# Kernel optimization log

Measured on AMD Instinct MI355X. Metric: run time of the kernel, lower is better.

The kernel has to match this reference:

```python
import jax, jax.numpy as jnp
import numpy as np

EPS = 1e-5
N, K, C = 200000, 9, 64  # active sites, 3x3 kernel offsets, channels


def setup_inputs() -> dict:
    key = jax.random.key(0)
    ks = jax.random.split(key, 4)
    x = jax.random.normal(ks[0], (N, C), dtype=jnp.float32)
    # rulebook: neighbor index per active site per kernel offset (submanifold conv)
    nbr = jax.random.randint(ks[1], (N, K), 0, N, dtype=jnp.int32)
    W1 = jax.random.normal(ks[2], (K, C, C), dtype=jnp.float32) * 0.05
    W2 = jax.random.normal(ks[3], (K, C, C), dtype=jnp.float32) * 0.05
    ones = jnp.ones((C,), dtype=jnp.float32)
    zeros = jnp.zeros((C,), dtype=jnp.float32)
    return {
        'x': x, 'nbr': nbr,
        'W1': W1, 'g1': ones, 'b1': zeros, 'rm1': zeros, 'rv1': ones,
        'W2': W2, 'g2': ones, 'b2': zeros, 'rm2': zeros, 'rv2': ones,
    }


def _subm_conv(f, nbr, W):
    # gather neighbor features [N, K, C] then contract with [K, C, C]
    return jnp.einsum('nkc,kcd->nd', f[nbr], W)


def _bn(a, g, b, rm, rv):
    inv = g * jax.lax.rsqrt(rv + EPS)
    return a * inv + (b - rm * inv)


def reference(x, nbr, W1, g1, b1, rm1, rv1, W2, g2, b2, rm2, rv2):
    a = _subm_conv(x, nbr, W1)
    a = jax.nn.relu(_bn(a, g1, b1, rm1, rv1))
    a = _subm_conv(a, nbr, W2)
    a = _bn(a, g2, b2, rm2, rv2)
    return jax.nn.relu(a + x)
```

## Files before the change

### kernel.cpp

```cpp
#include <hip/hip_runtime.h>

#define EPS 1e-5f

typedef unsigned short ushort;
typedef unsigned int uint;
typedef __attribute__((ext_vector_type(8)))  short  short8;
typedef __attribute__((ext_vector_type(8)))  ushort ushort8;
typedef __attribute__((ext_vector_type(16))) float  f32x16;

__device__ __forceinline__ ushort f2bf(float v) {
    uint b = __float_as_uint(v);
    return (ushort)((b + 0x7fffu + ((b >> 16) & 1u)) >> 16);
}
__device__ __forceinline__ float bf2f(ushort u) {
    return __uint_as_float(((uint)u) << 16);
}

__global__ void prep_w(const float* __restrict__ W,
                       ushort* __restrict__ hi, ushort* __restrict__ lo) {
    int e = blockIdx.x * 256 + threadIdx.x;
    int c = e & 63, d = (e >> 6) & 63, k = e >> 12;
    float v = W[(k << 12) + (c << 6) + d];
    ushort h = f2bf(v);
    hi[e] = h;
    lo[e] = f2bf(v - bf2f(h));
}

template<bool SECOND>
__global__ __launch_bounds__(256, 4) void subm_conv_mfma(
    const float*  __restrict__ f,
    const int*    __restrict__ nbr,
    const ushort* __restrict__ Wth,
    const ushort* __restrict__ Wtl,
    const float*  __restrict__ gamma,
    const float*  __restrict__ beta,
    const float*  __restrict__ rmean,
    const float*  __restrict__ rvar,
    const float*  __restrict__ resid,
    float* __restrict__ out)
{
    __shared__ __align__(16) ushort Ah[64][72];
    __shared__ __align__(16) ushort Al[64][72];
    __shared__ __align__(16) ushort Bh[64][72];
    __shared__ __align__(16) ushort Bl[64][72];

    const int t    = threadIdx.x;
    const int lane = t & 63;
    const int w    = t >> 6;
    const int wr   = (w >> 1) << 5;
    const int wc   = (w & 1) << 5;
    const int row0 = blockIdx.x << 6;

    const int sr = t >> 2;
    const int sc = (t & 3) << 4;

    f32x16 acc = 0.f;

    const int rA   = wr + (lane & 31);
    const int rB   = wc + (lane & 31);
    const int koff = (lane >> 5) << 3;

    for (int k = 0; k < 9; ++k) {
        const int m = nbr[(row0 + sr) * 9 + k];
        const float4* ap = (const float4*)(f + (size_t)m * 64 + sc);
        float4 v0 = ap[0], v1 = ap[1], v2 = ap[2], v3 = ap[3];

        const int woff = (k << 12) + (sr << 6) + sc;
        const uint4* whp = (const uint4*)(Wth + woff);
        const uint4* wlp = (const uint4*)(Wtl + woff);
        uint4 wh0 = whp[0], wh1 = whp[1];
        uint4 wl0 = wlp[0], wl1 = wlp[1];

        float a0[8] = {v0.x,v0.y,v0.z,v0.w, v1.x,v1.y,v1.z,v1.w};
        float a1[8] = {v2.x,v2.y,v2.z,v2.w, v3.x,v3.y,v3.z,v3.w};
        ushort8 h0, l0, h1, l1;
        #pragma unroll
        for (int j = 0; j < 8; ++j) {
            ushort h = f2bf(a0[j]);
            h0[j] = h; l0[j] = f2bf(a0[j] - bf2f(h));
            ushort g = f2bf(a1[j]);
            h1[j] = g; l1[j] = f2bf(a1[j] - bf2f(g));
        }

        __syncthreads();

        *(ushort8*)&Ah[sr][sc]     = h0;
        *(ushort8*)&Al[sr][sc]     = l0;
        *(ushort8*)&Ah[sr][sc + 8] = h1;
        *(ushort8*)&Al[sr][sc + 8] = l1;
        *(uint4*)&Bh[sr][sc]       = wh0;
        *(uint4*)&Bh[sr][sc + 8]   = wh1;
        *(uint4*)&Bl[sr][sc]       = wl0;
        *(uint4*)&Bl[sr][sc + 8]   = wl1;

        __syncthreads();

        #pragma unroll
        for (int h = 0; h < 4; ++h) {
            const int co = (h << 4) + koff;
            short8 fah = *(const short8*)&Ah[rA][co];
            short8 fal = *(const short8*)&Al[rA][co];
            short8 fbh = *(const short8*)&Bh[rB][co];
            short8 fbl = *(const short8*)&Bl[rB][co];
            acc = __builtin_amdgcn_mfma_f32_32x32x16_bf16(fah, fbh, acc, 0, 0, 0);
            acc = __builtin_amdgcn_mfma_f32_32x32x16_bf16(fah, fbl, acc, 0, 0, 0);
            acc = __builtin_amdgcn_mfma_f32_32x32x16_bf16(fal, fbh, acc, 0, 0, 0);
        }
    }

    const int d   = wc + (lane & 31);
    const float iv  = gamma[d] * rsqrtf(rvar[d] + EPS);
    const float add = beta[d] - rmean[d] * iv;
    const int rb  = row0 + wr + ((lane >> 5) << 2);
    #pragma unroll
    for (int i = 0; i < 16; ++i) {
        const int n = rb + (i & 3) + ((i >> 2) << 3);
        float val = fmaf(acc[i], iv, add);
        if (SECOND) val += resid[(size_t)n * 64 + d];
        out[(size_t)n * 64 + d] = fmaxf(val, 0.f);
    }
}

extern "C" void kernel_launch(void* const* d_in, const int* in_sizes, int n_in,
                              void* d_out, int out_size, void* d_ws, size_t ws_size,
                              hipStream_t stream) {
    const float* x   = (const float*)d_in[0];
    const int*   nbr = (const int*)  d_in[1];
    const float* W1  = (const float*)d_in[2];
    const float* g1  = (const float*)d_in[3];
    const float* b1  = (const float*)d_in[4];
    const float* rm1 = (const float*)d_in[5];
    const float* rv1 = (const float*)d_in[6];
    const float* W2  = (const float*)d_in[7];
    const float* g2  = (const float*)d_in[8];
    const float* b2  = (const float*)d_in[9];
    const float* rm2 = (const float*)d_in[10];
    const float* rv2 = (const float*)d_in[11];

    const int N    = in_sizes[0] / 64;
    const int grid = N / 64;

    char* ws = (char*)d_ws;
    float*  mid  = (float*)ws;                         ws += (size_t)N * 64 * 4;
    ushort* W1h  = (ushort*)ws;                        ws += 9 * 64 * 64 * 2;
    ushort* W1l  = (ushort*)ws;                        ws += 9 * 64 * 64 * 2;
    ushort* W2h  = (ushort*)ws;                        ws += 9 * 64 * 64 * 2;
    ushort* W2l  = (ushort*)ws;

    prep_w<<<144, 256, 0, stream>>>(W1, W1h, W1l);
    prep_w<<<144, 256, 0, stream>>>(W2, W2h, W2l);

    subm_conv_mfma<false><<<grid, 256, 0, stream>>>(
        x,   nbr, W1h, W1l, g1, b1, rm1, rv1, nullptr, mid);
    subm_conv_mfma<true ><<<grid, 256, 0, stream>>>(
        mid, nbr, W2h, W2l, g2, b2, rm2, rv2, x, (float*)d_out);
}
```

Baseline: 273.1 us.

## Pre-swizzle weights into MFMA fragment order and load B directly from global

The weight prep kernel now writes the bf16 hi/lo weights in the exact per-lane MFMA B-fragment order, and both weight tensors are prepared in one launch. The conv kernel drops the B tiles from shared memory and reads its B fragments straight from global/L2 with 16-byte loads, which halves LDS usage and removes the weight staging stores. Launch bounds rise from 4 to 8 blocks per CU to use the freed LDS for occupancy. In exchange the MFMA loop now waits on global loads of weights, which should stay cache-resident, and register pressure under the tighter bound may force spills.

```diff
diff --git a/kernel.cpp b/kernel.cpp
--- a/kernel.cpp
+++ b/kernel.cpp
@@ -16,22 +16,28 @@
     return __uint_as_float(((uint)u) << 16);
 }
 
-__global__ void prep_w(const float* __restrict__ W,
-                       ushort* __restrict__ hi, ushort* __restrict__ lo) {
+__global__ void prep_w2(const float* __restrict__ W1, const float* __restrict__ W2,
+                        ushort* __restrict__ h1, ushort* __restrict__ l1,
+                        ushort* __restrict__ h2, ushort* __restrict__ l2) {
     int e = blockIdx.x * 256 + threadIdx.x;
-    int c = e & 63, d = (e >> 6) & 63, k = e >> 12;
-    float v = W[(k << 12) + (c << 6) + d];
-    ushort h = f2bf(v);
-    hi[e] = h;
-    lo[e] = f2bf(v - bf2f(h));
+    const float* W = W1; ushort* ho = h1; ushort* lo = l1;
+    if (e >= 36864) { e -= 36864; W = W2; ho = h2; lo = l2; }
+    const int j = e & 7, l = (e >> 3) & 63, h = (e >> 9) & 3,
+              wc2 = (e >> 11) & 1, k = e >> 12;
+    const int d = wc2 * 32 + (l & 31);
+    const int c = h * 16 + ((l >> 5) << 3) + j;
+    const float v = W[(k << 12) + (c << 6) + d];
+    const ushort hh = f2bf(v);
+    ho[e] = hh;
+    lo[e] = f2bf(v - bf2f(hh));
 }
 
 template<bool SECOND>
-__global__ __launch_bounds__(256, 4) void subm_conv_mfma(
+__global__ __launch_bounds__(256, 8) void subm_conv_mfma(
     const float*  __restrict__ f,
     const int*    __restrict__ nbr,
-    const ushort* __restrict__ Wth,
-    const ushort* __restrict__ Wtl,
+    const ushort* __restrict__ Wfh,
+    const ushort* __restrict__ Wfl,
     const float*  __restrict__ gamma,
     const float*  __restrict__ beta,
     const float*  __restrict__ rmean,
@@ -41,14 +47,12 @@
 {
     __shared__ __align__(16) ushort Ah[64][72];
     __shared__ __align__(16) ushort Al[64][72];
-    __shared__ __align__(16) ushort Bh[64][72];
-    __shared__ __align__(16) ushort Bl[64][72];
 
     const int t    = threadIdx.x;
     const int lane = t & 63;
     const int w    = t >> 6;
     const int wr   = (w >> 1) << 5;
-    const int wc   = (w & 1) << 5;
+    const int wc2  = w & 1;
     const int row0 = blockIdx.x << 6;
 
     const int sr = t >> 2;
@@ -57,19 +61,12 @@
     f32x16 acc = 0.f;
 
     const int rA   = wr + (lane & 31);
-    const int rB   = wc + (lane & 31);
     const int koff = (lane >> 5) << 3;
 
     for (int k = 0; k < 9; ++k) {
         const int m = nbr[(row0 + sr) * 9 + k];
         const float4* ap = (const float4*)(f + (size_t)m * 64 + sc);
         float4 v0 = ap[0], v1 = ap[1], v2 = ap[2], v3 = ap[3];
-
-        const int woff = (k << 12) + (sr << 6) + sc;
-        const uint4* whp = (const uint4*)(Wth + woff);
-        const uint4* wlp = (const uint4*)(Wtl + woff);
-        uint4 wh0 = whp[0], wh1 = whp[1];
-        uint4 wl0 = wlp[0], wl1 = wlp[1];
 
         float a0[8] = {v0.x,v0.y,v0.z,v0.w, v1.x,v1.y,v1.z,v1.w};
         float a1[8] = {v2.x,v2.y,v2.z,v2.w, v3.x,v3.y,v3.z,v3.w};
@@ -88,30 +85,28 @@
         *(ushort8*)&Al[sr][sc]     = l0;
         *(ushort8*)&Ah[sr][sc + 8] = h1;
         *(ushort8*)&Al[sr][sc + 8] = l1;
-        *(uint4*)&Bh[sr][sc]       = wh0;
-        *(uint4*)&Bh[sr][sc + 8]   = wh1;
-        *(uint4*)&Bl[sr][sc]       = wl0;
-        *(uint4*)&Bl[sr][sc + 8]   = wl1;
 
         __syncthreads();
 
+        const ushort* bh = Wfh + (((k * 2 + wc2) * 4) * 64 + lane) * 8;
+        const ushort* bl = Wfl + (((k * 2 + wc2) * 4) * 64 + lane) * 8;
         #pragma unroll
         for (int h = 0; h < 4; ++h) {
             const int co = (h << 4) + koff;
             short8 fah = *(const short8*)&Ah[rA][co];
             short8 fal = *(const short8*)&Al[rA][co];
-            short8 fbh = *(const short8*)&Bh[rB][co];
-            short8 fbl = *(const short8*)&Bl[rB][co];
+            short8 fbh = *(const short8*)(bh + (h << 9));
+            short8 fbl = *(const short8*)(bl + (h << 9));
             acc = __builtin_amdgcn_mfma_f32_32x32x16_bf16(fah, fbh, acc, 0, 0, 0);
             acc = __builtin_amdgcn_mfma_f32_32x32x16_bf16(fah, fbl, acc, 0, 0, 0);
             acc = __builtin_amdgcn_mfma_f32_32x32x16_bf16(fal, fbh, acc, 0, 0, 0);
         }
     }
 
-    const int d   = wc + (lane & 31);
+    const int d     = (wc2 << 5) + (lane & 31);
     const float iv  = gamma[d] * rsqrtf(rvar[d] + EPS);
     const float add = beta[d] - rmean[d] * iv;
-    const int rb  = row0 + wr + ((lane >> 5) << 2);
+    const int rb    = row0 + wr + ((lane >> 5) << 2);
     #pragma unroll
     for (int i = 0; i < 16; ++i) {
         const int n = rb + (i & 3) + ((i >> 2) << 3);
@@ -141,14 +136,13 @@
     const int grid = N / 64;
 
     char* ws = (char*)d_ws;
-    float*  mid  = (float*)ws;                         ws += (size_t)N * 64 * 4;
-    ushort* W1h  = (ushort*)ws;                        ws += 9 * 64 * 64 * 2;
-    ushort* W1l  = (ushort*)ws;                        ws += 9 * 64 * 64 * 2;
-    ushort* W2h  = (ushort*)ws;                        ws += 9 * 64 * 64 * 2;
-    ushort* W2l  = (ushort*)ws;
+    float*  mid = (float*)ws;            ws += (size_t)N * 64 * 4;
+    ushort* W1h = (ushort*)ws;           ws += 36864 * 2;
+    ushort* W1l = (ushort*)ws;           ws += 36864 * 2;
+    ushort* W2h = (ushort*)ws;           ws += 36864 * 2;
+    ushort* W2l = (ushort*)ws;
 
-    prep_w<<<144, 256, 0, stream>>>(W1, W1h, W1l);
-    prep_w<<<144, 256, 0, stream>>>(W2, W2h, W2l);
+    prep_w2<<<288, 256, 0, stream>>>(W1, W2, W1h, W1l, W2h, W2l);
 
     subm_conv_mfma<false><<<grid, 256, 0, stream>>>(
         x,   nbr, W1h, W1l, g1, b1, rm1, rv1, nullptr, mid);
```

New measurement: 290.2 us. +6.3%, slower.
